# Kernel tuning notes

Hardware: AMD Instinct MI355X
Metric: run time of the kernel (lower is better)

## Reference

```python
import jax, jax.numpy as jnp
import numpy as np

NUM_CAPSULE = 5
DIM_CAPSULE = 5
ROUTINGS = 4
T_EPSILON = 1e-07


def squash(x, axis=-1):
    # Note: this module's 'squash' is pure norm-normalization (no v^2/(1+v^2) factor)
    s_squared_norm = jnp.sum(x * x, axis=axis, keepdims=True)
    return x / jnp.sqrt(s_squared_norm + T_EPSILON)


def setup_inputs() -> dict:
    key = jax.random.key(0)
    k1, k2 = jax.random.split(key)
    batch, seq, d_in = 1024, 512, 120
    x = jax.random.normal(k1, (batch, seq, d_in), dtype=jnp.float32)
    # xavier_normal for fan_in=120, fan_out=25
    std = float(np.sqrt(2.0 / (d_in + NUM_CAPSULE * DIM_CAPSULE)))
    W = jax.random.normal(k2, (1, d_in, NUM_CAPSULE * DIM_CAPSULE), dtype=jnp.float32) * std
    return {"x": x, "W": W}


def reference(x, W):
    batch, inp, _ = x.shape
    # u_hat_vecs: [batch, num_capsule, input_num_capsule, dim_capsule]
    u_hat = jnp.matmul(x, W[0])  # [b, inp, 25]
    u_hat = u_hat.reshape(batch, inp, NUM_CAPSULE, DIM_CAPSULE).transpose(0, 2, 1, 3)
    b = jnp.zeros((batch, NUM_CAPSULE, inp), dtype=u_hat.dtype)
    outputs = None
    for i in range(ROUTINGS):
        # torch code softmaxes over the num_capsule axis (dim 1 of b)
        c = jax.nn.softmax(b, axis=1)  # [b, ncaps, inp]
        outputs = squash(jnp.einsum('bij,bijk->bik', c, u_hat))  # [b, ncaps, dcap]
        if i < ROUTINGS - 1:
            b = jnp.einsum('bik,bijk->bij', outputs, u_hat)
    return outputs
```

## Files before the change

### kernel.cpp

```cpp
#include <hip/hip_runtime.h>


#define NCAP 5
#define DCAP 5
#define NOUT 25
#define DIN 120
#define SEQ 512
#define ROUTINGS 4

#define KT    12
#define LROW  513

__global__ __launch_bounds__(256) void caps_kernel(
    const float* __restrict__ x,
    const float* __restrict__ W,
    float* __restrict__ out)
{
    const int b    = blockIdx.x;
    const int t    = threadIdx.x;
    const int lane = t & 63;
    const int wv   = t >> 6;

    __shared__ float xt[KT * LROW];
    __shared__ float red[4][NOUT];

    const float* xb = x + (size_t)b * SEQ * DIN;

    float acc[2][NOUT];
#pragma unroll
    for (int r = 0; r < 2; ++r)
#pragma unroll
        for (int j = 0; j < NOUT; ++j) acc[r][j] = 0.f;

    for (int tile = 0; tile < 10; ++tile) {
        const int k0 = tile * KT;

#pragma unroll
        for (int i = 0; i < 6; ++i) {
            int f   = t + 256 * i;
            int row = f / 3;
            int q   = f - row * 3;
            float4 v = *(const float4*)(xb + row * DIN + k0 + 4 * q);
            xt[(4 * q + 0) * LROW + row] = v.x;
            xt[(4 * q + 1) * LROW + row] = v.y;
            xt[(4 * q + 2) * LROW + row] = v.z;
            xt[(4 * q + 3) * LROW + row] = v.w;
        }
        __syncthreads();

#pragma unroll
        for (int k = 0; k < KT; ++k) {
            float a  = xt[k * LROW + t];
            float bv = xt[k * LROW + t + 256];
            const float* wr = W + (k0 + k) * NOUT;
#pragma unroll
            for (int j = 0; j < NOUT; ++j) {
                float w = wr[j];
                acc[0][j] = fmaf(a,  w, acc[0][j]);
                acc[1][j] = fmaf(bv, w, acc[1][j]);
            }
        }
        __syncthreads();
    }

    float bb[2][NCAP];
#pragma unroll
    for (int r = 0; r < 2; ++r)
#pragma unroll
        for (int c = 0; c < NCAP; ++c) bb[r][c] = 0.f;

    float o[NOUT];

    for (int it = 0; it < ROUTINGS; ++it) {
        float p[NOUT];
#pragma unroll
        for (int j = 0; j < NOUT; ++j) p[j] = 0.f;

#pragma unroll
        for (int r = 0; r < 2; ++r) {
            float m = bb[r][0];
#pragma unroll
            for (int c = 1; c < NCAP; ++c) m = fmaxf(m, bb[r][c]);
            float e[NCAP]; float se = 0.f;
#pragma unroll
            for (int c = 0; c < NCAP; ++c) { e[c] = __expf(bb[r][c] - m); se += e[c]; }
            float inv = 1.f / se;
#pragma unroll
            for (int c = 0; c < NCAP; ++c) {
                float cc = e[c] * inv;
#pragma unroll
                for (int k = 0; k < DCAP; ++k)
                    p[c*DCAP + k] = fmaf(cc, acc[r][c*DCAP + k], p[c*DCAP + k]);
            }
        }

#pragma unroll
        for (int d = 1; d < 64; d <<= 1)
#pragma unroll
            for (int j = 0; j < NOUT; ++j) p[j] += __shfl_xor(p[j], d, 64);

        if (lane == 0) {
#pragma unroll
            for (int j = 0; j < NOUT; ++j) red[wv][j] = p[j];
        }
        __syncthreads();
        float s[NOUT];
#pragma unroll
        for (int j = 0; j < NOUT; ++j)
            s[j] = red[0][j] + red[1][j] + red[2][j] + red[3][j];
        __syncthreads();

#pragma unroll
        for (int c = 0; c < NCAP; ++c) {
            float ss = 0.f;
#pragma unroll
            for (int k = 0; k < DCAP; ++k)
                ss = fmaf(s[c*DCAP + k], s[c*DCAP + k], ss);
            float sc = rsqrtf(ss + 1e-7f);
#pragma unroll
            for (int k = 0; k < DCAP; ++k) o[c*DCAP + k] = s[c*DCAP + k] * sc;
        }

        if (it < ROUTINGS - 1) {
#pragma unroll
            for (int r = 0; r < 2; ++r)
#pragma unroll
                for (int c = 0; c < NCAP; ++c) {
                    float d0 = 0.f;
#pragma unroll
                    for (int k = 0; k < DCAP; ++k)
                        d0 = fmaf(o[c*DCAP + k], acc[r][c*DCAP + k], d0);
                    bb[r][c] = d0;
                }
        }
    }

    if (t < NOUT) out[(size_t)b * NOUT + t] = o[t];
}

extern "C" void kernel_launch(void* const* d_in, const int* in_sizes, int n_in,
                              void* d_out, int out_size, void* d_ws, size_t ws_size,
                              hipStream_t stream) {
    const float* x   = (const float*)d_in[0];
    const float* W   = (const float*)d_in[1];
    float*       o   = (float*)d_out;
    const int batch  = in_sizes[0] / (SEQ * DIN);
    caps_kernel<<<dim3(batch), dim3(256), 0, stream>>>(x, W, o);
}
```

Baseline: 407.6 us.

## Double-buffer x tiles with async global-to-LDS loads and float4 LDS reads

The x tile staging now uses __builtin_amdgcn_global_load_lds into one of two LDS buffers, so the next tile's load overlaps compute on the current one instead of stalling on a load-then-sync per tile. The LDS layout changes from a transposed, padded layout to row-major (12 floats per row). Each thread now reads its rows as float4 and does four FMAs per W element group. The cost is double the LDS footprint, which may limit blocks per CU, and the strided float4 LDS reads may cause bank conflicts. Correctness also depends on the async loads having completed before the barrier.

```diff
diff --git a/kernel.cpp b/kernel.cpp
--- a/kernel.cpp
+++ b/kernel.cpp
@@ -9,7 +9,11 @@
 #define ROUTINGS 4
 
 #define KT    12
-#define LROW  513
+#define NTILE 10
+#define BUFF  (SEQ * KT)
+
+typedef __attribute__((address_space(3))) void        as3_void;
+typedef const __attribute__((address_space(1))) void  as1_void;
 
 __global__ __launch_bounds__(256) void caps_kernel(
     const float* __restrict__ x,
@@ -21,7 +25,7 @@
     const int lane = t & 63;
     const int wv   = t >> 6;
 
-    __shared__ float xt[KT * LROW];
+    __shared__ float xt[2][BUFF];
     __shared__ float red[4][NOUT];
 
     const float* xb = x + (size_t)b * SEQ * DIN;
@@ -32,32 +36,43 @@
 #pragma unroll
         for (int j = 0; j < NOUT; ++j) acc[r][j] = 0.f;
 
-    for (int tile = 0; tile < 10; ++tile) {
+    auto stage = [&](int bufi, int tile) {
         const int k0 = tile * KT;
-
 #pragma unroll
         for (int i = 0; i < 6; ++i) {
-            int f   = t + 256 * i;
-            int row = f / 3;
-            int q   = f - row * 3;
-            float4 v = *(const float4*)(xb + row * DIN + k0 + 4 * q);
-            xt[(4 * q + 0) * LROW + row] = v.x;
-            xt[(4 * q + 1) * LROW + row] = v.y;
-            xt[(4 * q + 2) * LROW + row] = v.z;
-            xt[(4 * q + 3) * LROW + row] = v.w;
+            unsigned f   = (unsigned)t + 256u * (unsigned)i;
+            unsigned row = f / 3u;
+            unsigned q   = f - row * 3u;
+            const float* gsrc = xb + row * DIN + k0 + 4u * q;
+            float*      ldst = &xt[bufi][1024 * i + 256 * wv];
+            __builtin_amdgcn_global_load_lds((as1_void*)gsrc, (as3_void*)ldst,
+                                             16, 0, 0);
         }
-        __syncthreads();
+    };
 
+    stage(0, 0);
+    __syncthreads();
+
+    for (int tile = 0; tile < NTILE; ++tile) {
+        const int cur = tile & 1;
+        if (tile + 1 < NTILE) stage(cur ^ 1, tile + 1);
+
+        const int k0 = tile * KT;
+        const float* r0 = &xt[cur][t * KT];
+        const float* r1 = &xt[cur][(t + 256) * KT];
 #pragma unroll
-        for (int k = 0; k < KT; ++k) {
-            float a  = xt[k * LROW + t];
-            float bv = xt[k * LROW + t + 256];
-            const float* wr = W + (k0 + k) * NOUT;
+        for (int q = 0; q < 3; ++q) {
+            float4 a  = *(const float4*)(r0 + 4 * q);
+            float4 bv = *(const float4*)(r1 + 4 * q);
+            const float* wr = W + (k0 + 4 * q) * NOUT;
 #pragma unroll
             for (int j = 0; j < NOUT; ++j) {
-                float w = wr[j];
-                acc[0][j] = fmaf(a,  w, acc[0][j]);
-                acc[1][j] = fmaf(bv, w, acc[1][j]);
+                float w0 = wr[j];
+                float w1 = wr[j + NOUT];
+                float w2 = wr[j + 2 * NOUT];
+                float w3 = wr[j + 3 * NOUT];
+                acc[0][j] = fmaf(a.w,  w3, fmaf(a.z,  w2, fmaf(a.y,  w1, fmaf(a.x,  w0, acc[0][j]))));
+                acc[1][j] = fmaf(bv.w, w3, fmaf(bv.z, w2, fmaf(bv.y, w1, fmaf(bv.x, w0, acc[1][j]))));
             }
         }
         __syncthreads();
```

New measurement: 404.2 us. Within noise of the previous version (-0.8%).
